# Kernel tuning notes

Hardware: AMD Instinct MI355X
Metric: run time of the kernel (lower is better)

Reference implementation:

```python
import jax, jax.numpy as jnp
from jax import lax
import numpy as np

C_IN = 64
C_OUT = 64
CQ = C_OUT // 8   # query/key channels
K = 5             # axial kernel length
RATIO = 0.7       # hybrid-norm mixing ratio
EPS = 1e-5
DN = ('NCHW', 'OIHW', 'NCHW')


def setup_inputs() -> dict:
    key = jax.random.key(0)
    ks = jax.random.split(key, 16)
    rn = lambda k, s, sc=0.05: jax.random.normal(k, s, dtype=jnp.float32) * sc
    return dict(
        x=jax.random.normal(ks[0], (4, C_IN, 256, 256), dtype=jnp.float32),
        hconv_w=rn(ks[1], (C_IN, 1, 1, K)), hconv_b=rn(ks[2], (C_IN,)),
        vconv_w=rn(ks[3], (C_IN, 1, K, 1)), vconv_b=rn(ks[4], (C_IN,)),
        pw_w=rn(ks[5], (C_OUT, C_IN)), pw_b=rn(ks[6], (C_OUT,)),
        bn_w=1.0 + rn(ks[7], (C_OUT,)), bn_b=rn(ks[8], (C_OUT,)),
        q_w=rn(ks[9], (CQ, C_OUT)), q_b=rn(ks[10], (CQ,)),
        k_w=rn(ks[11], (CQ, C_OUT)), k_b=rn(ks[12], (CQ,)),
        v_w=rn(ks[13], (C_OUT, C_OUT)), v_b=rn(ks[14], (C_OUT,)),
        gamma=rn(ks[15], (1,), 0.1),
    )


def reference(x, hconv_w, hconv_b, vconv_w, vconv_b, pw_w, pw_b,
              bn_w, bn_b, q_w, q_b, k_w, k_b, v_w, v_b, gamma):
    # ---- AxialDepthwiseConv: depthwise (1,K) + (K,1) + x, relu, pointwise ----
    h = lax.conv_general_dilated(x, hconv_w, (1, 1), [(0, 0), (K // 2, K // 2)],
                                 dimension_numbers=DN, feature_group_count=C_IN)
    h = h + hconv_b[:, None, None]
    v = lax.conv_general_dilated(x, vconv_w, (1, 1), [(K // 2, K // 2), (0, 0)],
                                 dimension_numbers=DN, feature_group_count=C_IN)
    v = v + vconv_b[:, None, None]
    a = jax.nn.relu(h + v + x)
    y = jnp.einsum('bchw,oc->bohw', a, pw_w) + pw_b[:, None, None]

    # ---- HybridNormalization: 0.7*InstanceNorm(no affine) + 0.3*BatchNorm(train) ----
    im = y.mean((2, 3), keepdims=True)
    iv = y.var((2, 3), keepdims=True)
    inn = (y - im) * lax.rsqrt(iv + EPS)
    bm = y.mean((0, 2, 3), keepdims=True)
    bv = y.var((0, 2, 3), keepdims=True)
    bnn = (y - bm) * lax.rsqrt(bv + EPS) * bn_w[:, None, None] + bn_b[:, None, None]
    y = RATIO * inn + (1.0 - RATIO) * bnn

    # ---- CrissCrossAttention ----
    q = jnp.einsum('bchw,oc->bohw', y, q_w) + q_b[:, None, None]   # (B,CQ,H,W)
    k = jnp.einsum('bchw,oc->bohw', y, k_w) + k_b[:, None, None]   # (B,CQ,H,W)
    val = jnp.einsum('bchw,oc->bohw', y, v_w) + v_b[:, None, None] # (B,C,H,W)

    # height (per column w): attn[b,w,j,i] = softmax_i( q[b,:,j,w] . k[b,:,i,w] )
    Ah = jax.nn.softmax(jnp.einsum('bcjw,bciw->bwji', q, k), axis=-1)
    # h_out[b,c,i,w] = sum_j val[b,c,j,w] * Ah[b,w,j,i]  (matches bmm(value, attn))
    h_out = jnp.einsum('bcjw,bwji->bciw', val, Ah)

    # width (per row h): attn[b,h,y,x] = softmax_x( q[b,:,h,y] . k[b,:,h,x] )
    Av = jax.nn.softmax(jnp.einsum('bchy,bchx->bhyx', q, k), axis=-1)
    v_out = jnp.einsum('bchy,bhyx->bchx', val, Av)

    out = gamma[0] * (h_out + v_out) + y

    # ---- MaxPool2d(2,2) ----
    down = lax.reduce_window(out, -jnp.inf, lax.max, (1, 1, 2, 2), (1, 1, 2, 2), 'VALID')
    return out, down
```

## Files before the change

kernel.cpp:

```cpp
#include <hip/hip_runtime.h>
#include <hip/hip_bf16.h>

#define Bn 4
#define Cc 64
#define CQn 8
#define Hh 256
#define Ww 256
#define PLANE 65536

typedef unsigned short ushortT;
typedef __attribute__((ext_vector_type(8))) unsigned short us8;
typedef __attribute__((ext_vector_type(4))) unsigned short us4;
typedef __attribute__((ext_vector_type(8))) __bf16 bf16x8;
typedef __attribute__((ext_vector_type(4))) float f32x4;

__device__ inline ushortT f2bf(float f) {
    __hip_bfloat16 h = __float2bfloat16(f);
    return *(ushortT*)&h;
}
__device__ inline float bf2f(ushortT u) {
    return __uint_as_float((unsigned)u << 16);
}
union BF8U { us8 u; bf16x8 b; uint4 w; };
__device__ inline us8 zero_us8() {
    BF8U z; z.w.x = 0; z.w.y = 0; z.w.z = 0; z.w.w = 0; return z.u;
}

__global__ void pack_weights_kernel(
    const float* __restrict__ pww, const float* __restrict__ qw,
    const float* __restrict__ kw, const float* __restrict__ vw,
    ushortT* __restrict__ pw_bf, ushortT* __restrict__ qk_bf,
    ushortT* __restrict__ vw_bf)
{
    int i = blockIdx.x * 256 + threadIdx.x;
    if (i < 64 * 64) pw_bf[i] = f2bf(pww[i]);
    if (i < 64 * 64) vw_bf[i] = f2bf(vw[i]);
    if (i < 8 * 64)  qk_bf[i] = f2bf(qw[i]);
    if (i >= 8 * 64 && i < 16 * 64) qk_bf[i] = f2bf(kw[i - 512]);
}

__global__ __launch_bounds__(256) void dw_kernel(
    const float* __restrict__ x,
    const float* __restrict__ hw, const float* __restrict__ hb,
    const float* __restrict__ vw, const float* __restrict__ vb,
    ushortT* __restrict__ aout)
{
    int blk = blockIdx.x;
    int bc = blk >> 4;
    int ht = blk & 15;
    int h0 = ht * 16;
    int c = bc & 63;
    int tid = threadIdx.x;
    __shared__ float rows[20][260];
    const float* xp = x + (size_t)bc * PLANE;
    #pragma unroll
    for (int i = 0; i < 20; ++i) {
        int hr = h0 - 2 + i;
        rows[i][tid + 2] = (hr >= 0 && hr < Hh) ? xp[hr * Ww + tid] : 0.f;
    }
    if (tid < 20) {
        rows[tid][0] = 0.f; rows[tid][1] = 0.f;
        rows[tid][258] = 0.f; rows[tid][259] = 0.f;
    }
    __syncthreads();

    float hw0 = hw[c * 5 + 0], hw1 = hw[c * 5 + 1], hw2 = hw[c * 5 + 2],
          hw3 = hw[c * 5 + 3], hw4 = hw[c * 5 + 4];
    float vw0 = vw[c * 5 + 0], vw1 = vw[c * 5 + 1], vw2 = vw[c * 5 + 2],
          vw3 = vw[c * 5 + 3], vw4 = vw[c * 5 + 4];
    float bias = hb[c] + vb[c];

    ushortT* op = aout + (size_t)bc * PLANE + h0 * Ww + tid;
    #pragma unroll
    for (int r = 0; r < 16; ++r) {
        float hs = hw0 * rows[r + 2][tid]     + hw1 * rows[r + 2][tid + 1]
                 + hw2 * rows[r + 2][tid + 2] + hw3 * rows[r + 2][tid + 3]
                 + hw4 * rows[r + 2][tid + 4];
        float vs = vw0 * rows[r][tid + 2]     + vw1 * rows[r + 1][tid + 2]
                 + vw2 * rows[r + 2][tid + 2] + vw3 * rows[r + 3][tid + 2]
                 + vw4 * rows[r + 4][tid + 2];
        float res = hs + vs + bias + rows[r + 2][tid + 2];
        op[r * Ww] = f2bf(fmaxf(res, 0.f));
    }
}

__global__ __launch_bounds__(256) void pw_mfma_kernel(
    const ushortT* __restrict__ a_bf, const ushortT* __restrict__ pw_bf,
    const float* __restrict__ pwb,
    float* __restrict__ y_raw, float* __restrict__ sums, float* __restrict__ sumsq)
{
    int blk = blockIdx.x;
    int b = blk >> 8;
    int t0 = (blk & 255) << 8;
    int tid = threadIdx.x, lane = tid & 63, wv = tid >> 6;
    int half = lane >> 4;
    int col = lane & 15;

    __shared__ ushortT ytile[256 * 74];

    {
        size_t base = (size_t)b * Cc * PLANE + t0 + tid;
        uint* wrow = (uint*)&ytile[tid * 74];
        #pragma unroll
        for (int c = 0; c < Cc; c += 2) {
            ushortT v0 = a_bf[base + (size_t)c * PLANE];
            ushortT v1 = a_bf[base + (size_t)(c + 1) * PLANE];
            wrow[c >> 1] = (uint)v0 | ((uint)v1 << 16);
        }
    }
    __syncthreads();

    int m0 = wv * 16;
    BF8U a0, a1;
    a0.u = *(const us8*)(pw_bf + (m0 + col) * 64 + half * 8);
    a1.u = *(const us8*)(pw_bf + (m0 + col) * 64 + 32 + half * 8);

    float bias[4], s[4], s2[4];
    #pragma unroll
    for (int r = 0; r < 4; ++r) {
        bias[r] = pwb[m0 + half * 4 + r];
        s[r] = 0.f; s2[r] = 0.f;
    }

    const uint* lw = (const uint*)ytile;
    #pragma unroll 4
    for (int t = 0; t < 16; ++t) {
        int rbase = (t * 16 + col) * 37 + half * 4;
        BF8U b0, b1;
        b0.w.x = lw[rbase];      b0.w.y = lw[rbase + 1];
        b0.w.z = lw[rbase + 2];  b0.w.w = lw[rbase + 3];
        b1.w.x = lw[rbase + 16]; b1.w.y = lw[rbase + 17];
        b1.w.z = lw[rbase + 18]; b1.w.w = lw[rbase + 19];
        f32x4 acc = (f32x4){0.f, 0.f, 0.f, 0.f};
        acc = __builtin_amdgcn_mfma_f32_16x16x32_bf16(a0.b, b0.b, acc, 0, 0, 0);
        acc = __builtin_amdgcn_mfma_f32_16x16x32_bf16(a1.b, b1.b, acc, 0, 0, 0);
        int pix = t * 16 + col;
        #pragma unroll
        for (int r = 0; r < 4; ++r) {
            int c = m0 + half * 4 + r;
            float v = acc[r] + bias[r];
            y_raw[(size_t)(b * Cc + c) * PLANE + t0 + pix] = v;
            s[r] += v; s2[r] += v * v;
        }
    }
    #pragma unroll
    for (int r = 0; r < 4; ++r) {
        #pragma unroll
        for (int d = 8; d > 0; d >>= 1) {
            s[r]  += __shfl_down(s[r], d, 16);
            s2[r] += __shfl_down(s2[r], d, 16);
        }
    }
    if (col == 0) {
        #pragma unroll
        for (int r = 0; r < 4; ++r) {
            int c = m0 + half * 4 + r;
            atomicAdd(&sums[b * Cc + c], s[r]);
            atomicAdd(&sumsq[b * Cc + c], s2[r]);
        }
    }
}

__global__ void finalize_kernel(
    const float* __restrict__ sums, const float* __restrict__ sumsq,
    const float* __restrict__ bn_w, const float* __restrict__ bn_b,
    float* __restrict__ alpha, float* __restrict__ beta)
{
    int c = threadIdx.x;
    if (c >= Cc) return;
    float im[4], e2[4];
    float bm = 0.f, be2 = 0.f;
    for (int b = 0; b < 4; ++b) {
        im[b] = sums[b * Cc + c] * (1.f / 65536.f);
        e2[b] = sumsq[b * Cc + c] * (1.f / 65536.f);
        bm += im[b]; be2 += e2[b];
    }
    bm *= 0.25f; be2 *= 0.25f;
    float bv = be2 - bm * bm;
    float rsb = rsqrtf(bv + 1e-5f);
    float wgt = bn_w[c], bb = bn_b[c];
    for (int b = 0; b < 4; ++b) {
        float iv = e2[b] - im[b] * im[b];
        float rsi = rsqrtf(iv + 1e-5f);
        float al = 0.7f * rsi + 0.3f * rsb * wgt;
        float bt = -0.7f * im[b] * rsi - 0.3f * bm * rsb * wgt + 0.3f * bb;
        alpha[b * Cc + c] = al;
        beta[b * Cc + c] = bt;
    }
}

__global__ __launch_bounds__(256) void qkv_mfma_kernel(
    const float* __restrict__ y_raw,
    const float* __restrict__ alpha, const float* __restrict__ beta,
    const ushortT* __restrict__ qk_bf, const float* __restrict__ qbias,
    const float* __restrict__ kbias,
    const ushortT* __restrict__ vw_bf, const float* __restrict__ vbias,
    float* __restrict__ y_norm, ushortT* __restrict__ q, ushortT* __restrict__ k,
    ushortT* __restrict__ val)
{
    int blk = blockIdx.x;
    int b = blk >> 8;
    int t0 = (blk & 255) << 8;
    int tid = threadIdx.x, lane = tid & 63, wv = tid >> 6;
    int half = lane >> 4;
    int col = lane & 15;

    __shared__ ushortT ytile[256 * 74];

    {
        size_t base = (size_t)b * Cc * PLANE + t0 + tid;
        uint* wrow = (uint*)&ytile[tid * 74];
        #pragma unroll
        for (int c = 0; c < Cc; c += 2) {
            float v0 = y_raw[base + (size_t)c * PLANE];
            float v1 = y_raw[base + (size_t)(c + 1) * PLANE];
            float n0 = alpha[b * Cc + c] * v0 + beta[b * Cc + c];
            float n1 = alpha[b * Cc + c + 1] * v1 + beta[b * Cc + c + 1];
            y_norm[base + (size_t)c * PLANE] = n0;
            y_norm[base + (size_t)(c + 1) * PLANE] = n1;
            wrow[c >> 1] = (uint)f2bf(n0) | ((uint)f2bf(n1) << 16);
        }
    }
    __syncthreads();

    const uint* lw = (const uint*)ytile;

    {
        BF8U a0, a1;
        a0.u = *(const us8*)(qk_bf + col * 64 + half * 8);
        a1.u = *(const us8*)(qk_bf + col * 64 + 32 + half * 8);
        #pragma unroll
        for (int i = 0; i < 4; ++i) {
            int t = wv * 4 + i;
            int rbase = (t * 16 + col) * 37 + half * 4;
            BF8U b0, b1;
            b0.w.x = lw[rbase];      b0.w.y = lw[rbase + 1];
            b0.w.z = lw[rbase + 2];  b0.w.w = lw[rbase + 3];
            b1.w.x = lw[rbase + 16]; b1.w.y = lw[rbase + 17];
            b1.w.z = lw[rbase + 18]; b1.w.w = lw[rbase + 19];
            f32x4 acc = (f32x4){0.f, 0.f, 0.f, 0.f};
            acc = __builtin_amdgcn_mfma_f32_16x16x32_bf16(a0.b, b0.b, acc, 0, 0, 0);
            acc = __builtin_amdgcn_mfma_f32_16x16x32_bf16(a1.b, b1.b, acc, 0, 0, 0);
            int pix = t * 16 + col;
            #pragma unroll
            for (int r = 0; r < 4; ++r) {
                int row = half * 4 + r;
                if (row < 8)
                    q[(size_t)(b * CQn + row) * PLANE + t0 + pix] = f2bf(acc[r] + qbias[row]);
                else
                    k[(size_t)(b * CQn + row - 8) * PLANE + t0 + pix] = f2bf(acc[r] + kbias[row - 8]);
            }
        }
    }

    {
        int m0 = wv * 16;
        BF8U a0, a1;
        a0.u = *(const us8*)(vw_bf + (m0 + col) * 64 + half * 8);
        a1.u = *(const us8*)(vw_bf + (m0 + col) * 64 + 32 + half * 8);
        float bias[4];
        #pragma unroll
        for (int r = 0; r < 4; ++r) bias[r] = vbias[m0 + half * 4 + r];
        #pragma unroll 4
        for (int t = 0; t < 16; ++t) {
            int rbase = (t * 16 + col) * 37 + half * 4;
            BF8U b0, b1;
            b0.w.x = lw[rbase];      b0.w.y = lw[rbase + 1];
            b0.w.z = lw[rbase + 2];  b0.w.w = lw[rbase + 3];
            b1.w.x = lw[rbase + 16]; b1.w.y = lw[rbase + 17];
            b1.w.z = lw[rbase + 18]; b1.w.w = lw[rbase + 19];
            f32x4 acc = (f32x4){0.f, 0.f, 0.f, 0.f};
            acc = __builtin_amdgcn_mfma_f32_16x16x32_bf16(a0.b, b0.b, acc, 0, 0, 0);
            acc = __builtin_amdgcn_mfma_f32_16x16x32_bf16(a1.b, b1.b, acc, 0, 0, 0);
            int pix = t * 16 + col;
            #pragma unroll
            for (int r = 0; r < 4; ++r) {
                int c = m0 + half * 4 + r;
                val[(size_t)(b * Cc + c) * PLANE + t0 + pix] = f2bf(acc[r] + bias[r]);
            }
        }
    }
}

__global__ __launch_bounds__(256) void transpose16_kernel(
    const ushortT* __restrict__ src, ushortT* __restrict__ dst)
{
    int blk = blockIdx.x;
    int plane = blk >> 6;
    int tile = blk & 63;
    int th = (tile >> 3) * 32;
    int tw = (tile & 7) * 32;
    __shared__ ushortT t[32][34];
    const ushortT* s = src + (size_t)plane * PLANE;
    ushortT* d = dst + (size_t)plane * PLANE;
    int lw = threadIdx.x & 31;
    int lh = threadIdx.x >> 5;
    #pragma unroll
    for (int i = 0; i < 4; ++i)
        t[lh + 8 * i][lw] = s[(th + lh + 8 * i) * Ww + tw + lw];
    __syncthreads();
    #pragma unroll
    for (int i = 0; i < 4; ++i)
        d[(tw + lh + 8 * i) * Hh + th + lw] = t[lw][lh + 8 * i];
}

template<bool BF16OUT>
__global__ __launch_bounds__(256) void attn_mfma2_kernel(
    const ushortT* __restrict__ q, const ushortT* __restrict__ k,
    const ushortT* __restrict__ val, void* __restrict__ outp)
{
    int blk = blockIdx.x;
    int b = blk >> 8;
    int r = blk & 255;
    int tid = threadIdx.x;
    int lane = tid & 63;
    int wv = tid >> 6;
    int col = lane & 15;
    int quad = lane >> 4;

    __shared__ ushortT q_s[256 * 8];
    __shared__ ushortT k_s[256 * 8];
    __shared__ ushortT val_lds[64 * 264];
    __shared__ ushortT A_lds[256 * 4 * 8];
    __shared__ float mhat[256];
    __shared__ float shiftv[256];
    __shared__ float kred[32];

    size_t qkbase = (size_t)b * CQn * PLANE + (size_t)r * Ww + tid;
    float qf[8], ka[8];
    {
        BF8U qp, kp;
        #pragma unroll
        for (int c = 0; c < 8; ++c) {
            ushortT qv = q[qkbase + (size_t)c * PLANE];
            ushortT kv = k[qkbase + (size_t)c * PLANE];
            qp.u[c] = qv; kp.u[c] = kv;
            qf[c] = bf2f(qv);
            ka[c] = fabsf(bf2f(kv));
        }
        *(us8*)&q_s[tid * 8] = qp.u;
        *(us8*)&k_s[tid * 8] = kp.u;
    }
    #pragma unroll
    for (int d = 1; d < 64; d <<= 1)
        #pragma unroll
        for (int c = 0; c < 8; ++c)
            ka[c] = fmaxf(ka[c], __shfl_xor(ka[c], d));
    if (lane == 0)
        #pragma unroll
        for (int c = 0; c < 8; ++c) kred[wv * 8 + c] = ka[c];

    size_t vbase = (size_t)b * Cc * PLANE + (size_t)r * Ww;
    {
        int c = tid >> 2, sub = tid & 3;
        #pragma unroll
        for (int p = 0; p < 8; ++p) {
            int j0 = (p * 4 + sub) * 8;
            us8 v = *(const us8*)(val + vbase + (size_t)c * PLANE + j0);
            *(us8*)&val_lds[c * 264 + j0] = v;
        }
    }
    __syncthreads();

    {
        float mh = 0.f;
        #pragma unroll
        for (int c = 0; c < 8; ++c) {
            float km = fmaxf(fmaxf(kred[c], kred[8 + c]),
                             fmaxf(kred[16 + c], kred[24 + c]));
            mh += fabsf(qf[c]) * km;
        }
        mhat[tid] = mh;
    }
    __syncthreads();

    #pragma unroll
    for (int t = 0; t < 4; ++t) {
        int jt = wv * 4 + t;
        BF8U qa; qa.u = zero_us8();
        if (quad == 0) qa.u = *(const us8*)&q_s[(jt * 16 + col) * 8];
        float mh4[4];
        #pragma unroll
        for (int rr = 0; rr < 4; ++rr) mh4[rr] = mhat[jt * 16 + quad * 4 + rr];
        f32x4 ls = (f32x4){0.f, 0.f, 0.f, 0.f};
        for (int it = 0; it < 16; ++it) {
            BF8U kb; kb.u = zero_us8();
            if (quad == 0) kb.u = *(const us8*)&k_s[(it * 16 + col) * 8];
            f32x4 sacc = (f32x4){0.f, 0.f, 0.f, 0.f};
            sacc = __builtin_amdgcn_mfma_f32_16x16x32_bf16(qa.b, kb.b, sacc, 0, 0, 0);
            #pragma unroll
            for (int rr = 0; rr < 4; ++rr)
                ls[rr] += __expf(sacc[rr] - mh4[rr]);
        }
        #pragma unroll
        for (int d = 1; d < 16; d <<= 1)
            #pragma unroll
            for (int rr = 0; rr < 4; ++rr)
                ls[rr] += __shfl_xor(ls[rr], d);
        if (col == 0)
            #pragma unroll
            for (int rr = 0; rr < 4; ++rr)
                shiftv[jt * 16 + quad * 4 + rr] = mh4[rr] + __logf(ls[rr]);
    }
    __syncthreads();

    BF8U kc[4];
    #pragma unroll
    for (int i = 0; i < 4; ++i) {
        kc[i].u = zero_us8();
        if (quad == 0) kc[i].u = *(const us8*)&k_s[((wv * 4 + i) * 16 + col) * 8];
    }
    f32x4 acc[16];
    #pragma unroll
    for (int t = 0; t < 16; ++t) acc[t] = (f32x4){0.f, 0.f, 0.f, 0.f};

    for (int ks = 0; ks < 8; ++ks) {
        #pragma unroll
        for (int jj2 = 0; jj2 < 2; ++jj2) {
            int jt = ks * 2 + jj2;
            BF8U qa; qa.u = zero_us8();
            if (quad == 0) qa.u = *(const us8*)&q_s[(jt * 16 + col) * 8];
            float sh4[4];
            #pragma unroll
            for (int rr = 0; rr < 4; ++rr) sh4[rr] = shiftv[jt * 16 + quad * 4 + rr];
            #pragma unroll
            for (int i = 0; i < 4; ++i) {
                f32x4 sacc = (f32x4){0.f, 0.f, 0.f, 0.f};
                sacc = __builtin_amdgcn_mfma_f32_16x16x32_bf16(qa.b, kc[i].b, sacc, 0, 0, 0);
                us4 pk;
                #pragma unroll
                for (int rr = 0; rr < 4; ++rr)
                    pk[rr] = f2bf(__expf(sacc[rr] - sh4[rr]));
                int irow = (wv * 4 + i) * 16 + col;
                int jq = jj2 * 2 + (quad >> 1);
                *(us4*)&A_lds[(irow * 4 + jq) * 8 + (quad & 1) * 4] = pk;
            }
        }
        __syncthreads();
        BF8U af;
        af.u = *(const us8*)&val_lds[(wv * 16 + col) * 264 + ks * 32 + quad * 8];
        #pragma unroll
        for (int t = 0; t < 16; ++t) {
            BF8U bfr;
            bfr.u = *(const us8*)&A_lds[((t * 16 + col) * 4 + quad) * 8];
            acc[t] = __builtin_amdgcn_mfma_f32_16x16x32_bf16(af.b, bfr.b, acc[t], 0, 0, 0);
        }
        __syncthreads();
    }

    size_t obase = (size_t)b * Cc * PLANE + (size_t)r * Ww;
    #pragma unroll
    for (int t = 0; t < 16; ++t) {
        int i = t * 16 + col;
        #pragma unroll
        for (int rr = 0; rr < 4; ++rr) {
            int c = wv * 16 + quad * 4 + rr;
            float v = acc[t][rr];
            size_t addr = obase + (size_t)c * PLANE + i;
            if (BF16OUT) ((ushortT*)outp)[addr] = f2bf(v);
            else         ((float*)outp)[addr] = v;
        }
    }
}

__global__ __launch_bounds__(256) void final_kernel(
    const ushortT* __restrict__ houtT, const float* __restrict__ y_norm,
    const float* __restrict__ gamma,
    float* __restrict__ out, float* __restrict__ down)
{
    int blk = blockIdx.x;
    int tile = blk & 63;
    int bc = blk >> 6;
    int th = (tile >> 3) * 32;
    int tw = (tile & 7) * 32;
    __shared__ float t[32][33];
    const ushortT* hT = houtT + (size_t)bc * PLANE;
    {
        int ww = threadIdx.x >> 3;
        int hh = (threadIdx.x & 7) * 4;
        us4 v4 = *(const us4*)(hT + (size_t)(tw + ww) * Hh + th + hh);
        t[hh + 0][ww] = __uint_as_float((unsigned)v4[0] << 16);
        t[hh + 1][ww] = __uint_as_float((unsigned)v4[1] << 16);
        t[hh + 2][ww] = __uint_as_float((unsigned)v4[2] << 16);
        t[hh + 3][ww] = __uint_as_float((unsigned)v4[3] << 16);
    }
    __syncthreads();
    float g = gamma[0];
    int qw_ = threadIdx.x & 15;
    int qh_ = threadIdx.x >> 4;
    const float* yb = y_norm + (size_t)bc * PLANE;
    float* ob = out + (size_t)bc * PLANE;
    float mx = -1e30f;
    float2 res[2];
    #pragma unroll
    for (int i = 0; i < 2; ++i) {
        int hh = 2 * qh_ + i;
        int off = (th + hh) * Ww + tw + 2 * qw_;
        float2 v = *(const float2*)(ob + off);
        float2 y = *(const float2*)(yb + off);
        float o0 = g * (t[hh][2 * qw_]     + v.x) + y.x;
        float o1 = g * (t[hh][2 * qw_ + 1] + v.y) + y.y;
        res[i] = make_float2(o0, o1);
        mx = fmaxf(mx, fmaxf(o0, o1));
    }
    #pragma unroll
    for (int i = 0; i < 2; ++i) {
        int off = (th + 2 * qh_ + i) * Ww + tw + 2 * qw_;
        *(float2*)(ob + off) = res[i];
    }
    down[(size_t)bc * 16384 + (th / 2 + qh_) * 128 + tw / 2 + qw_] = mx;
}

extern "C" void kernel_launch(void* const* d_in, const int* in_sizes, int n_in,
                              void* d_out, int out_size, void* d_ws, size_t ws_size,
                              hipStream_t stream)
{
    const float* x     = (const float*)d_in[0];
    const float* hw    = (const float*)d_in[1];
    const float* hb    = (const float*)d_in[2];
    const float* vw    = (const float*)d_in[3];
    const float* vb    = (const float*)d_in[4];
    const float* pww   = (const float*)d_in[5];
    const float* pwb   = (const float*)d_in[6];
    const float* bnw   = (const float*)d_in[7];
    const float* bnb   = (const float*)d_in[8];
    const float* qw    = (const float*)d_in[9];
    const float* qb    = (const float*)d_in[10];
    const float* kw    = (const float*)d_in[11];
    const float* kb    = (const float*)d_in[12];
    const float* vw2   = (const float*)d_in[13];
    const float* vb2   = (const float*)d_in[14];
    const float* gamma = (const float*)d_in[15];

    float* ws = (float*)d_ws;
    const size_t NP = (size_t)Bn * Cc * PLANE;
    const size_t NQ = (size_t)Bn * CQn * PLANE;
    float* y_raw  = ws;
    float* y_norm = ws + NP;
    float* slotC  = ws + 2 * NP;
    float* slotD  = ws + 2 * NP + NP / 2;
    float* ptr    = ws + 3 * NP;
    ushortT* qbuf = (ushortT*)ptr;
    ushortT* kbuf = qbuf + NQ;
    ushortT* qT   = kbuf + NQ;
    ushortT* kT   = qT + NQ;
    float* sums   = (float*)(kT + NQ);
    float* sumsq  = sums + 256;
    float* alpha  = sumsq + 256;
    float* beta   = alpha + 256;
    ushortT* pw_bf = (ushortT*)(beta + 256);
    ushortT* qk_bf = pw_bf + 64 * 64;
    ushortT* vw_bf = qk_bf + 16 * 64;

    ushortT* a_buf = (ushortT*)slotC;
    ushortT* valT  = (ushortT*)slotC;
    ushortT* valb  = (ushortT*)slotD;
    ushortT* houtT = (ushortT*)slotD;
    float* out  = (float*)d_out;
    float* down = out + NP;

    hipMemsetAsync(sums, 0, 512 * sizeof(float), stream);
    pack_weights_kernel<<<dim3(16), dim3(256), 0, stream>>>(
        pww, qw, kw, vw2, pw_bf, qk_bf, vw_bf);
    dw_kernel<<<dim3(Bn * Cc * 16), dim3(256), 0, stream>>>(
        x, hw, hb, vw, vb, a_buf);
    pw_mfma_kernel<<<dim3(Bn * 256), dim3(256), 0, stream>>>(
        a_buf, pw_bf, pwb, y_raw, sums, sumsq);
    finalize_kernel<<<dim3(1), dim3(64), 0, stream>>>(
        sums, sumsq, bnw, bnb, alpha, beta);
    qkv_mfma_kernel<<<dim3(Bn * 256), dim3(256), 0, stream>>>(
        y_raw, alpha, beta, qk_bf, qb, kb, vw_bf, vb2,
        y_norm, qbuf, kbuf, valb);
    transpose16_kernel<<<dim3(Bn * CQn * 64), dim3(256), 0, stream>>>(qbuf, qT);
    transpose16_kernel<<<dim3(Bn * CQn * 64), dim3(256), 0, stream>>>(kbuf, kT);
    transpose16_kernel<<<dim3(Bn * Cc * 64), dim3(256), 0, stream>>>(valb, valT);
    attn_mfma2_kernel<false><<<dim3(Bn * Hh), dim3(256), 0, stream>>>(
        qbuf, kbuf, valb, (void*)out);
    attn_mfma2_kernel<true><<<dim3(Bn * Hh), dim3(256), 0, stream>>>(
        qT, kT, valT, (void*)houtT);
    final_kernel<<<dim3(Bn * Cc * 64), dim3(256), 0, stream>>>(
        houtT, y_norm, gamma, out, down);
}
```

Measured before the change: 426.8 us.

## Merge transposes and both attention passes, fold finalize into qkv, stream V from global

```diff
diff --git a/kernel.cpp b/kernel.cpp
--- a/kernel.cpp
+++ b/kernel.cpp
@@ -161,37 +161,10 @@
     }
 }
 
-__global__ void finalize_kernel(
-    const float* __restrict__ sums, const float* __restrict__ sumsq,
-    const float* __restrict__ bn_w, const float* __restrict__ bn_b,
-    float* __restrict__ alpha, float* __restrict__ beta)
-{
-    int c = threadIdx.x;
-    if (c >= Cc) return;
-    float im[4], e2[4];
-    float bm = 0.f, be2 = 0.f;
-    for (int b = 0; b < 4; ++b) {
-        im[b] = sums[b * Cc + c] * (1.f / 65536.f);
-        e2[b] = sumsq[b * Cc + c] * (1.f / 65536.f);
-        bm += im[b]; be2 += e2[b];
-    }
-    bm *= 0.25f; be2 *= 0.25f;
-    float bv = be2 - bm * bm;
-    float rsb = rsqrtf(bv + 1e-5f);
-    float wgt = bn_w[c], bb = bn_b[c];
-    for (int b = 0; b < 4; ++b) {
-        float iv = e2[b] - im[b] * im[b];
-        float rsi = rsqrtf(iv + 1e-5f);
-        float al = 0.7f * rsi + 0.3f * rsb * wgt;
-        float bt = -0.7f * im[b] * rsi - 0.3f * bm * rsb * wgt + 0.3f * bb;
-        alpha[b * Cc + c] = al;
-        beta[b * Cc + c] = bt;
-    }
-}
-
 __global__ __launch_bounds__(256) void qkv_mfma_kernel(
     const float* __restrict__ y_raw,
-    const float* __restrict__ alpha, const float* __restrict__ beta,
+    const float* __restrict__ sums, const float* __restrict__ sumsq,
+    const float* __restrict__ bnw, const float* __restrict__ bnb,
     const ushortT* __restrict__ qk_bf, const float* __restrict__ qbias,
     const float* __restrict__ kbias,
     const ushortT* __restrict__ vw_bf, const float* __restrict__ vbias,
@@ -206,6 +179,26 @@
     int col = lane & 15;
 
     __shared__ ushortT ytile[256 * 74];
+    __shared__ float alpha_s[64], beta_s[64];
+
+    if (tid < 64) {
+        int c = tid;
+        float im[4], e2[4];
+        float bm = 0.f, be2 = 0.f;
+        #pragma unroll
+        for (int bb = 0; bb < 4; ++bb) {
+            im[bb] = sums[bb * Cc + c] * (1.f / 65536.f);
+            e2[bb] = sumsq[bb * Cc + c] * (1.f / 65536.f);
+            bm += im[bb]; be2 += e2[bb];
+        }
+        bm *= 0.25f; be2 *= 0.25f;
+        float rsb = rsqrtf(be2 - bm * bm + 1e-5f);
+        float wgt = bnw[c];
+        float rsi = rsqrtf(e2[b] - im[b] * im[b] + 1e-5f);
+        alpha_s[c] = 0.7f * rsi + 0.3f * rsb * wgt;
+        beta_s[c]  = -0.7f * im[b] * rsi - 0.3f * bm * rsb * wgt + 0.3f * bnb[c];
+    }
+    __syncthreads();
 
     {
         size_t base = (size_t)b * Cc * PLANE + t0 + tid;
@@ -214,8 +207,8 @@
         for (int c = 0; c < Cc; c += 2) {
             float v0 = y_raw[base + (size_t)c * PLANE];
             float v1 = y_raw[base + (size_t)(c + 1) * PLANE];
-            float n0 = alpha[b * Cc + c] * v0 + beta[b * Cc + c];
-            float n1 = alpha[b * Cc + c + 1] * v1 + beta[b * Cc + c + 1];
+            float n0 = alpha_s[c] * v0 + beta_s[c];
+            float n1 = alpha_s[c + 1] * v1 + beta_s[c + 1];
             y_norm[base + (size_t)c * PLANE] = n0;
             y_norm[base + (size_t)(c + 1) * PLANE] = n1;
             wrow[c >> 1] = (uint)f2bf(n0) | ((uint)f2bf(n1) << 16);
@@ -282,36 +275,47 @@
     }
 }
 
-__global__ __launch_bounds__(256) void transpose16_kernel(
-    const ushortT* __restrict__ src, ushortT* __restrict__ dst)
+__global__ __launch_bounds__(256) void transpose_all_kernel(
+    const ushortT* __restrict__ qb, ushortT* __restrict__ qT,
+    const ushortT* __restrict__ kb, ushortT* __restrict__ kT,
+    const ushortT* __restrict__ vb, ushortT* __restrict__ vT)
 {
     int blk = blockIdx.x;
     int plane = blk >> 6;
     int tile = blk & 63;
+    const ushortT* src; ushortT* dst;
+    if (plane < 32)      { src = qb + (size_t)plane * PLANE;        dst = qT + (size_t)plane * PLANE; }
+    else if (plane < 64) { src = kb + (size_t)(plane - 32) * PLANE; dst = kT + (size_t)(plane - 32) * PLANE; }
+    else                 { src = vb + (size_t)(plane - 64) * PLANE; dst = vT + (size_t)(plane - 64) * PLANE; }
     int th = (tile >> 3) * 32;
     int tw = (tile & 7) * 32;
     __shared__ ushortT t[32][34];
-    const ushortT* s = src + (size_t)plane * PLANE;
-    ushortT* d = dst + (size_t)plane * PLANE;
     int lw = threadIdx.x & 31;
     int lh = threadIdx.x >> 5;
     #pragma unroll
     for (int i = 0; i < 4; ++i)
-        t[lh + 8 * i][lw] = s[(th + lh + 8 * i) * Ww + tw + lw];
+        t[lh + 8 * i][lw] = src[(th + lh + 8 * i) * Ww + tw + lw];
     __syncthreads();
     #pragma unroll
     for (int i = 0; i < 4; ++i)
-        d[(tw + lh + 8 * i) * Hh + th + lw] = t[lw][lh + 8 * i];
-}
-
-template<bool BF16OUT>
-__global__ __launch_bounds__(256) void attn_mfma2_kernel(
-    const ushortT* __restrict__ q, const ushortT* __restrict__ k,
-    const ushortT* __restrict__ val, void* __restrict__ outp)
+        dst[(tw + lh + 8 * i) * Hh + th + lw] = t[lw][lh + 8 * i];
+}
+
+__global__ __launch_bounds__(256) void attn_kernel(
+    const ushortT* __restrict__ q0, const ushortT* __restrict__ k0,
+    const ushortT* __restrict__ v0, ushortT* __restrict__ o0,
+    const ushortT* __restrict__ q1, const ushortT* __restrict__ k1,
+    const ushortT* __restrict__ v1, ushortT* __restrict__ o1)
 {
     int blk = blockIdx.x;
-    int b = blk >> 8;
-    int r = blk & 255;
+    int sel = blk >> 10;
+    const ushortT* __restrict__ q   = sel ? q1 : q0;
+    const ushortT* __restrict__ k   = sel ? k1 : k0;
+    const ushortT* __restrict__ val = sel ? v1 : v0;
+    ushortT* __restrict__ outp      = sel ? o1 : o0;
+    int bblk = blk & 1023;
+    int b = bblk >> 8;
+    int r = bblk & 255;
     int tid = threadIdx.x;
     int lane = tid & 63;
     int wv = tid >> 6;
@@ -320,11 +324,15 @@
 
     __shared__ ushortT q_s[256 * 8];
     __shared__ ushortT k_s[256 * 8];
-    __shared__ ushortT val_lds[64 * 264];
-    __shared__ ushortT A_lds[256 * 4 * 8];
+    __shared__ ushortT A_lds[4 * 256 * 8];
     __shared__ float mhat[256];
     __shared__ float shiftv[256];
     __shared__ float kred[32];
+
+    size_t vbase = (size_t)b * Cc * PLANE + (size_t)r * Ww
+                 + (size_t)(wv * 16 + col) * PLANE + quad * 8;
+    BF8U afb[2];
+    afb[0].u = *(const us8*)(val + vbase);
 
     size_t qkbase = (size_t)b * CQn * PLANE + (size_t)r * Ww + tid;
     float qf[8], ka[8];
@@ -349,17 +357,6 @@
     if (lane == 0)
         #pragma unroll
         for (int c = 0; c < 8; ++c) kred[wv * 8 + c] = ka[c];
-
-    size_t vbase = (size_t)b * Cc * PLANE + (size_t)r * Ww;
-    {
-        int c = tid >> 2, sub = tid & 3;
-        #pragma unroll
-        for (int p = 0; p < 8; ++p) {
-            int j0 = (p * 4 + sub) * 8;
-            us8 v = *(const us8*)(val + vbase + (size_t)c * PLANE + j0);
-            *(us8*)&val_lds[c * 264 + j0] = v;
-        }
-    }
     __syncthreads();
 
     {
@@ -384,8 +381,8 @@
         for (int rr = 0; rr < 4; ++rr) mh4[rr] = mhat[jt * 16 + quad * 4 + rr];
         f32x4 ls = (f32x4){0.f, 0.f, 0.f, 0.f};
         for (int it = 0; it < 16; ++it) {
-            BF8U kb; kb.u = zero_us8();
-            if (quad == 0) kb.u = *(const us8*)&k_s[(it * 16 + col) * 8];
+            BF8U kb;
+            kb.u = *(const us8*)&k_s[(it * 16 + col) * 8];
             f32x4 sacc = (f32x4){0.f, 0.f, 0.f, 0.f};
             sacc = __builtin_amdgcn_mfma_f32_16x16x32_bf16(qa.b, kb.b, sacc, 0, 0, 0);
             #pragma unroll
@@ -406,15 +403,16 @@
 
     BF8U kc[4];
     #pragma unroll
-    for (int i = 0; i < 4; ++i) {
-        kc[i].u = zero_us8();
-        if (quad == 0) kc[i].u = *(const us8*)&k_s[((wv * 4 + i) * 16 + col) * 8];
-    }
+    for (int i = 0; i < 4; ++i)
+        kc[i].u = *(const us8*)&k_s[((wv * 4 + i) * 16 + col) * 8];
     f32x4 acc[16];
     #pragma unroll
     for (int t = 0; t < 16; ++t) acc[t] = (f32x4){0.f, 0.f, 0.f, 0.f};
 
+    #pragma unroll
     for (int ks = 0; ks < 8; ++ks) {
+        if (ks < 7)
+            afb[(ks + 1) & 1].u = *(const us8*)(val + vbase + (ks + 1) * 32);
         #pragma unroll
         for (int jj2 = 0; jj2 < 2; ++jj2) {
             int jt = ks * 2 + jj2;
@@ -433,17 +431,15 @@
                     pk[rr] = f2bf(__expf(sacc[rr] - sh4[rr]));
                 int irow = (wv * 4 + i) * 16 + col;
                 int jq = jj2 * 2 + (quad >> 1);
-                *(us4*)&A_lds[(irow * 4 + jq) * 8 + (quad & 1) * 4] = pk;
+                *(us4*)&A_lds[(jq * 256 + irow) * 8 + (quad & 1) * 4] = pk;
             }
         }
         __syncthreads();
-        BF8U af;
-        af.u = *(const us8*)&val_lds[(wv * 16 + col) * 264 + ks * 32 + quad * 8];
         #pragma unroll
         for (int t = 0; t < 16; ++t) {
             BF8U bfr;
-            bfr.u = *(const us8*)&A_lds[((t * 16 + col) * 4 + quad) * 8];
-            acc[t] = __builtin_amdgcn_mfma_f32_16x16x32_bf16(af.b, bfr.b, acc[t], 0, 0, 0);
+            bfr.u = *(const us8*)&A_lds[(quad * 256 + t * 16 + col) * 8];
+            acc[t] = __builtin_amdgcn_mfma_f32_16x16x32_bf16(afb[ks & 1].b, bfr.b, acc[t], 0, 0, 0);
         }
         __syncthreads();
     }
@@ -455,17 +451,14 @@
         #pragma unroll
         for (int rr = 0; rr < 4; ++rr) {
             int c = wv * 16 + quad * 4 + rr;
-            float v = acc[t][rr];
-            size_t addr = obase + (size_t)c * PLANE + i;
-            if (BF16OUT) ((ushortT*)outp)[addr] = f2bf(v);
-            else         ((float*)outp)[addr] = v;
+            outp[obase + (size_t)c * PLANE + i] = f2bf(acc[t][rr]);
         }
     }
 }
 
 __global__ __launch_bounds__(256) void final_kernel(
-    const ushortT* __restrict__ houtT, const float* __restrict__ y_norm,
-    const float* __restrict__ gamma,
+    const ushortT* __restrict__ houtT, const ushortT* __restrict__ hout0,
+    const float* __restrict__ y_norm, const float* __restrict__ gamma,
     float* __restrict__ out, float* __restrict__ down)
 {
     int blk = blockIdx.x;
@@ -489,6 +482,7 @@
     int qw_ = threadIdx.x & 15;
     int qh_ = threadIdx.x >> 4;
     const float* yb = y_norm + (size_t)bc * PLANE;
+    const ushortT* hb = hout0 + (size_t)bc * PLANE;
     float* ob = out + (size_t)bc * PLANE;
     float mx = -1e30f;
     float2 res[2];
@@ -496,10 +490,10 @@
     for (int i = 0; i < 2; ++i) {
         int hh = 2 * qh_ + i;
         int off = (th + hh) * Ww + tw + 2 * qw_;
-        float2 v = *(const float2*)(ob + off);
+        uint hv = *(const uint*)(hb + off);
         float2 y = *(const float2*)(yb + off);
-        float o0 = g * (t[hh][2 * qw_]     + v.x) + y.x;
-        float o1 = g * (t[hh][2 * qw_ + 1] + v.y) + y.y;
+        float o0 = g * (t[hh][2 * qw_]     + bf2f((ushortT)(hv & 0xffff))) + y.x;
+        float o1 = g * (t[hh][2 * qw_ + 1] + bf2f((ushortT)(hv >> 16)))   + y.y;
         res[i] = make_float2(o0, o1);
         mx = fmaxf(mx, fmaxf(o0, o1));
     }
@@ -546,16 +540,15 @@
     ushortT* kT   = qT + NQ;
     float* sums   = (float*)(kT + NQ);
     float* sumsq  = sums + 256;
-    float* alpha  = sumsq + 256;
-    float* beta   = alpha + 256;
-    ushortT* pw_bf = (ushortT*)(beta + 256);
+    ushortT* pw_bf = (ushortT*)(sumsq + 256);
     ushortT* qk_bf = pw_bf + 64 * 64;
     ushortT* vw_bf = qk_bf + 16 * 64;
 
     ushortT* a_buf = (ushortT*)slotC;
     ushortT* valT  = (ushortT*)slotC;
     ushortT* valb  = (ushortT*)slotD;
-    ushortT* houtT = (ushortT*)slotD;
+    ushortT* hout0 = (ushortT*)y_raw;
+    ushortT* houtT = hout0 + NP;
     float* out  = (float*)d_out;
     float* down = out + NP;
 
@@ -566,18 +559,13 @@
         x, hw, hb, vw, vb, a_buf);
     pw_mfma_kernel<<<dim3(Bn * 256), dim3(256), 0, stream>>>(
         a_buf, pw_bf, pwb, y_raw, sums, sumsq);
-    finalize_kernel<<<dim3(1), dim3(64), 0, stream>>>(
-        sums, sumsq, bnw, bnb, alpha, beta);
     qkv_mfma_kernel<<<dim3(Bn * 256), dim3(256), 0, stream>>>(
-        y_raw, alpha, beta, qk_bf, qb, kb, vw_bf, vb2,
+        y_raw, sums, sumsq, bnw, bnb, qk_bf, qb, kb, vw_bf, vb2,
         y_norm, qbuf, kbuf, valb);
-    transpose16_kernel<<<dim3(Bn * CQn * 64), dim3(256), 0, stream>>>(qbuf, qT);
-    transpose16_kernel<<<dim3(Bn * CQn * 64), dim3(256), 0, stream>>>(kbuf, kT);
-    transpose16_kernel<<<dim3(Bn * Cc * 64), dim3(256), 0, stream>>>(valb, valT);
-    attn_mfma2_kernel<false><<<dim3(Bn * Hh), dim3(256), 0, stream>>>(
-        qbuf, kbuf, valb, (void*)out);
-    attn_mfma2_kernel<true><<<dim3(Bn * Hh), dim3(256), 0, stream>>>(
-        qT, kT, valT, (void*)houtT);
+    transpose_all_kernel<<<dim3(320 * 64), dim3(256), 0, stream>>>(
+        qbuf, qT, kbuf, kT, valb, valT);
+    attn_kernel<<<dim3(2 * Bn * Hh), dim3(256), 0, stream>>>(
+        qbuf, kbuf, valb, hout0, qT, kT, valT, houtT);
     final_kernel<<<dim3(Bn * Cc * 64), dim3(256), 0, stream>>>(
-        houtT, y_norm, gamma, out, down);
-}
+        houtT, hout0, y_norm, gamma, out, down);
+}
```

Result: faster. 371.6 us (-12.9%).
